# Optimization experiments

Measured on AMD Instinct MI355X. Metric: run time of the kernel, lower is better.

## Reference

```python
import jax, jax.numpy as jnp
import numpy as np

DELTA = 1.0
CENSORING_WEIGHT = 1.0
N = 16777216  # batch_size


def setup_inputs() -> dict:
    key = jax.random.key(0)
    k1, k2, k3, k4, k5, k6 = jax.random.split(key, 6)
    return {
        "pred_ecoli": jax.random.normal(k1, (N,), dtype=jnp.float32),
        "pred_saureus": jax.random.normal(k2, (N,), dtype=jnp.float32),
        "targets": jax.random.normal(k3, (N,), dtype=jnp.float32),
        "bacteria_ids": jax.random.randint(k4, (N,), 0, 2, dtype=jnp.int32),
        "is_censored": jax.random.bernoulli(k5, 0.5, (N,)),
        "censoring_threshold": jax.random.normal(k6, (N,), dtype=jnp.float32),
    }


def _huber(pred, target, delta):
    abs_error = jnp.abs(pred - target)
    quadratic = jnp.minimum(abs_error, delta)  # clamp(max=delta)
    linear = abs_error - quadratic
    return 0.5 * quadratic ** 2 + delta * linear


def reference(pred_ecoli, pred_saureus, targets, bacteria_ids, is_censored, censoring_threshold):
    # head selection: bacteria_id == 0 -> E.coli head, else S.aureus head
    pred = jnp.where(bacteria_ids == 0, pred_ecoli, pred_saureus)
    # censored branch: clamp(threshold - pred, min=0)^2 * censoring_weight
    censored_loss = CENSORING_WEIGHT * jnp.maximum(censoring_threshold - pred, 0.0) ** 2
    huber = _huber(pred, targets, DELTA)
    per_sample = jnp.where(is_censored, censored_loss, huber)
    return jnp.mean(per_sample)
```

## Files before the change

### kernel.cpp

```cpp
#include <hip/hip_runtime.h>

#define NBLOCKS 2048
#define NTHREADS 256

__device__ __forceinline__ float per_sample(float pe, float ps, float tg,
                                            float th, int bid, int cen) {
  float pred = (bid == 0) ? pe : ps;
  float d = fmaxf(th - pred, 0.0f);
  float closs = d * d;
  float ae = fabsf(pred - tg);
  float q = fminf(ae, 1.0f);
  float hub = 0.5f * q * q + (ae - q);
  return cen ? closs : hub;
}

__global__ void detect_layout(const unsigned char* __restrict__ cens,
                              int* __restrict__ flag) {
  __shared__ int any;
  if (threadIdx.x == 0) any = 0;
  __syncthreads();
  int local = 0;
  for (int i = threadIdx.x; i < 4096; i += blockDim.x) {
    if ((i & 3) != 0 && cens[i] != 0) local = 1;
  }
  if (local) atomicOr(&any, 1);
  __syncthreads();
  if (threadIdx.x == 0) *flag = (any == 0) ? 1 : 0;
}

__device__ __forceinline__ float proc4(const float4& e, const float4& s,
                                       const float4& t, const float4& h,
                                       const int4& b, int c0, int c1, int c2,
                                       int c3) {
  float a = per_sample(e.x, s.x, t.x, h.x, b.x, c0);
  a += per_sample(e.y, s.y, t.y, h.y, b.y, c1);
  a += per_sample(e.z, s.z, t.z, h.z, b.z, c2);
  a += per_sample(e.w, s.w, t.w, h.w, b.w, c3);
  return a;
}

__global__ __launch_bounds__(NTHREADS, 8) void dualhead_loss_kernel(
    const float4* __restrict__ pe, const float4* __restrict__ ps,
    const float4* __restrict__ tg, const int4* __restrict__ bid,
    const void* __restrict__ cens, const float4* __restrict__ th,
    const int* __restrict__ flag, float* __restrict__ partials, int nvec) {
  const int is32 = *flag;
  float acc = 0.0f;
  const int stride = gridDim.x * blockDim.x;
  int i = blockIdx.x * blockDim.x + threadIdx.x;

  for (; i + stride < nvec; i += 2 * stride) {
    const int j = i + stride;
    float4 e0 = pe[i], e1 = pe[j];
    float4 s0 = ps[i], s1 = ps[j];
    float4 t0 = tg[i], t1 = tg[j];
    float4 h0 = th[i], h1 = th[j];
    int4 b0 = bid[i], b1 = bid[j];
    int c00, c01, c02, c03, c10, c11, c12, c13;
    if (is32) {
      int4 c0 = ((const int4*)cens)[i];
      int4 c1 = ((const int4*)cens)[j];
      c00 = c0.x; c01 = c0.y; c02 = c0.z; c03 = c0.w;
      c10 = c1.x; c11 = c1.y; c12 = c1.z; c13 = c1.w;
    } else {
      uchar4 c0 = ((const uchar4*)cens)[i];
      uchar4 c1 = ((const uchar4*)cens)[j];
      c00 = c0.x; c01 = c0.y; c02 = c0.z; c03 = c0.w;
      c10 = c1.x; c11 = c1.y; c12 = c1.z; c13 = c1.w;
    }
    acc += proc4(e0, s0, t0, h0, b0, c00, c01, c02, c03);
    acc += proc4(e1, s1, t1, h1, b1, c10, c11, c12, c13);
  }
  for (; i < nvec; i += stride) {
    float4 e = pe[i], s = ps[i], t = tg[i], h = th[i];
    int4 b = bid[i];
    int c0, c1, c2, c3;
    if (is32) {
      int4 c = ((const int4*)cens)[i];
      c0 = c.x; c1 = c.y; c2 = c.z; c3 = c.w;
    } else {
      uchar4 c = ((const uchar4*)cens)[i];
      c0 = c.x; c1 = c.y; c2 = c.z; c3 = c.w;
    }
    acc += proc4(e, s, t, h, b, c0, c1, c2, c3);
  }

  for (int off = 32; off > 0; off >>= 1) acc += __shfl_down(acc, off, 64);
  __shared__ float wsum[NTHREADS / 64];
  const int lane = threadIdx.x & 63;
  const int wid = threadIdx.x >> 6;
  if (lane == 0) wsum[wid] = acc;
  __syncthreads();
  if (threadIdx.x == 0) {
    float b = 0.0f;
    for (int w = 0; w < NTHREADS / 64; ++w) b += wsum[w];
    partials[blockIdx.x] = b;
  }
}

__global__ void final_reduce(const float* __restrict__ partials, int n,
                             float* __restrict__ out, double inv_n) {
  double acc = 0.0;
  for (int i = threadIdx.x; i < n; i += blockDim.x) acc += (double)partials[i];
  for (int off = 32; off > 0; off >>= 1) acc += __shfl_down(acc, off, 64);
  __shared__ double wsum[256 / 64];
  const int lane = threadIdx.x & 63;
  const int wid = threadIdx.x >> 6;
  if (lane == 0) wsum[wid] = acc;
  __syncthreads();
  if (threadIdx.x == 0) {
    double s = 0.0;
    for (int w = 0; w < 4; ++w) s += wsum[w];
    out[0] = (float)(s * inv_n);
  }
}

extern "C" void kernel_launch(void* const* d_in, const int* in_sizes, int n_in,
                              void* d_out, int out_size, void* d_ws, size_t ws_size,
                              hipStream_t stream) {
  const float* pe = (const float*)d_in[0];
  const float* ps = (const float*)d_in[1];
  const float* tg = (const float*)d_in[2];
  const int* bid = (const int*)d_in[3];
  const void* cens = d_in[4];
  const float* th = (const float*)d_in[5];
  const int n = in_sizes[0];
  const int nvec = n / 4;

  float* partials = (float*)d_ws;
  int* flag = (int*)((char*)d_ws + NBLOCKS * sizeof(float));

  detect_layout<<<1, 256, 0, stream>>>((const unsigned char*)cens, flag);
  dualhead_loss_kernel<<<NBLOCKS, NTHREADS, 0, stream>>>(
      (const float4*)pe, (const float4*)ps, (const float4*)tg,
      (const int4*)bid, cens, (const float4*)th, flag, partials, nvec);
  final_reduce<<<1, 256, 0, stream>>>(partials, NBLOCKS, (float*)d_out,
                                      1.0 / (double)n);
}
```

Measured before the change: 87.22 us.

## Fuse layout detection and final reduction into single streaming kernel

Removes the separate layout-detection and final-reduce kernel launches. Each wavefront now probes the first 256 bytes of the censoring mask with a ballot to infer whether it is byte or int32 encoded. Block partials are summed with a double atomicAdd and a last-block counter that writes the mean. A memset replaces the launch that reset the workspace. Risks include atomic contention across 2048 blocks and a heuristic probe over only 256 bytes.

```diff
diff --git a/kernel.cpp b/kernel.cpp
--- a/kernel.cpp
+++ b/kernel.cpp
@@ -14,20 +14,6 @@
   return cen ? closs : hub;
 }
 
-__global__ void detect_layout(const unsigned char* __restrict__ cens,
-                              int* __restrict__ flag) {
-  __shared__ int any;
-  if (threadIdx.x == 0) any = 0;
-  __syncthreads();
-  int local = 0;
-  for (int i = threadIdx.x; i < 4096; i += blockDim.x) {
-    if ((i & 3) != 0 && cens[i] != 0) local = 1;
-  }
-  if (local) atomicOr(&any, 1);
-  __syncthreads();
-  if (threadIdx.x == 0) *flag = (any == 0) ? 1 : 0;
-}
-
 __device__ __forceinline__ float proc4(const float4& e, const float4& s,
                                        const float4& t, const float4& h,
                                        const int4& b, int c0, int c1, int c2,
@@ -39,12 +25,15 @@
   return a;
 }
 
-__global__ __launch_bounds__(NTHREADS, 8) void dualhead_loss_kernel(
+__global__ __launch_bounds__(NTHREADS, 8) void dualhead_fused_kernel(
     const float4* __restrict__ pe, const float4* __restrict__ ps,
     const float4* __restrict__ tg, const int4* __restrict__ bid,
     const void* __restrict__ cens, const float4* __restrict__ th,
-    const int* __restrict__ flag, float* __restrict__ partials, int nvec) {
-  const int is32 = *flag;
+    double* __restrict__ accum, unsigned* __restrict__ counter,
+    float* __restrict__ out, int nvec, double inv_n) {
+  unsigned probe = ((const unsigned*)cens)[threadIdx.x & 63];
+  const bool is8 = __ballot((probe & 0xFFFFFF00u) != 0) != 0ULL;
+
   float acc = 0.0f;
   const int stride = gridDim.x * blockDim.x;
   int i = blockIdx.x * blockDim.x + threadIdx.x;
@@ -57,14 +46,14 @@
     float4 h0 = th[i], h1 = th[j];
     int4 b0 = bid[i], b1 = bid[j];
     int c00, c01, c02, c03, c10, c11, c12, c13;
-    if (is32) {
-      int4 c0 = ((const int4*)cens)[i];
-      int4 c1 = ((const int4*)cens)[j];
+    if (is8) {
+      uchar4 c0 = ((const uchar4*)cens)[i];
+      uchar4 c1 = ((const uchar4*)cens)[j];
       c00 = c0.x; c01 = c0.y; c02 = c0.z; c03 = c0.w;
       c10 = c1.x; c11 = c1.y; c12 = c1.z; c13 = c1.w;
     } else {
-      uchar4 c0 = ((const uchar4*)cens)[i];
-      uchar4 c1 = ((const uchar4*)cens)[j];
+      int4 c0 = ((const int4*)cens)[i];
+      int4 c1 = ((const int4*)cens)[j];
       c00 = c0.x; c01 = c0.y; c02 = c0.z; c03 = c0.w;
       c10 = c1.x; c11 = c1.y; c12 = c1.z; c13 = c1.w;
     }
@@ -75,11 +64,11 @@
     float4 e = pe[i], s = ps[i], t = tg[i], h = th[i];
     int4 b = bid[i];
     int c0, c1, c2, c3;
-    if (is32) {
-      int4 c = ((const int4*)cens)[i];
+    if (is8) {
+      uchar4 c = ((const uchar4*)cens)[i];
       c0 = c.x; c1 = c.y; c2 = c.z; c3 = c.w;
     } else {
-      uchar4 c = ((const uchar4*)cens)[i];
+      int4 c = ((const int4*)cens)[i];
       c0 = c.x; c1 = c.y; c2 = c.z; c3 = c.w;
     }
     acc += proc4(e, s, t, h, b, c0, c1, c2, c3);
@@ -91,27 +80,18 @@
   const int wid = threadIdx.x >> 6;
   if (lane == 0) wsum[wid] = acc;
   __syncthreads();
+
   if (threadIdx.x == 0) {
     float b = 0.0f;
     for (int w = 0; w < NTHREADS / 64; ++w) b += wsum[w];
-    partials[blockIdx.x] = b;
-  }
-}
-
-__global__ void final_reduce(const float* __restrict__ partials, int n,
-                             float* __restrict__ out, double inv_n) {
-  double acc = 0.0;
-  for (int i = threadIdx.x; i < n; i += blockDim.x) acc += (double)partials[i];
-  for (int off = 32; off > 0; off >>= 1) acc += __shfl_down(acc, off, 64);
-  __shared__ double wsum[256 / 64];
-  const int lane = threadIdx.x & 63;
-  const int wid = threadIdx.x >> 6;
-  if (lane == 0) wsum[wid] = acc;
-  __syncthreads();
-  if (threadIdx.x == 0) {
-    double s = 0.0;
-    for (int w = 0; w < 4; ++w) s += wsum[w];
-    out[0] = (float)(s * inv_n);
+    atomicAdd(accum, (double)b);
+    __threadfence();
+    unsigned t = atomicAdd(counter, 1u);
+    if (t == gridDim.x - 1) {
+      __threadfence();
+      double s = atomicAdd(accum, 0.0);
+      out[0] = (float)(s * inv_n);
+    }
   }
 }
 
@@ -127,13 +107,13 @@
   const int n = in_sizes[0];
   const int nvec = n / 4;
 
-  float* partials = (float*)d_ws;
-  int* flag = (int*)((char*)d_ws + NBLOCKS * sizeof(float));
+  double* accum = (double*)d_ws;
+  unsigned* counter = (unsigned*)((char*)d_ws + sizeof(double));
 
-  detect_layout<<<1, 256, 0, stream>>>((const unsigned char*)cens, flag);
-  dualhead_loss_kernel<<<NBLOCKS, NTHREADS, 0, stream>>>(
+  hipMemsetAsync(d_ws, 0, 16, stream);
+
+  dualhead_fused_kernel<<<NBLOCKS, NTHREADS, 0, stream>>>(
       (const float4*)pe, (const float4*)ps, (const float4*)tg,
-      (const int4*)bid, cens, (const float4*)th, flag, partials, nvec);
-  final_reduce<<<1, 256, 0, stream>>>(partials, NBLOCKS, (float*)d_out,
-                                      1.0 / (double)n);
+      (const int4*)bid, cens, (const float4*)th, accum, counter,
+      (float*)d_out, nvec, 1.0 / (double)n);
 }
```

After: 175.3 us. 101% more time.

## Fold layout detection into main kernel and use contiguous per-block chunks

Applied to the files above, without the earlier changes.

Drops the separate detect_layout launch. Each wavefront of the main kernel now reads the first 64 words of the censor mask and uses a ballot to decide whether it holds bytes or 32-bit values. The main loop also changes from a grid-stride pattern to a contiguous chunk per block, with a leftover loop for the remainder. This removes one kernel launch and its serialization, at the cost of a small redundant probe read in every wave and a 256-byte detection window instead of 4096 bytes.

```diff
diff --git a/kernel.cpp b/kernel.cpp
--- a/kernel.cpp
+++ b/kernel.cpp
@@ -14,20 +14,6 @@
   return cen ? closs : hub;
 }
 
-__global__ void detect_layout(const unsigned char* __restrict__ cens,
-                              int* __restrict__ flag) {
-  __shared__ int any;
-  if (threadIdx.x == 0) any = 0;
-  __syncthreads();
-  int local = 0;
-  for (int i = threadIdx.x; i < 4096; i += blockDim.x) {
-    if ((i & 3) != 0 && cens[i] != 0) local = 1;
-  }
-  if (local) atomicOr(&any, 1);
-  __syncthreads();
-  if (threadIdx.x == 0) *flag = (any == 0) ? 1 : 0;
-}
-
 __device__ __forceinline__ float proc4(const float4& e, const float4& s,
                                        const float4& t, const float4& h,
                                        const int4& b, int c0, int c1, int c2,
@@ -39,47 +25,65 @@
   return a;
 }
 
-__global__ __launch_bounds__(NTHREADS, 8) void dualhead_loss_kernel(
+__global__ __launch_bounds__(NTHREADS, 8) void dualhead_main(
     const float4* __restrict__ pe, const float4* __restrict__ ps,
     const float4* __restrict__ tg, const int4* __restrict__ bid,
     const void* __restrict__ cens, const float4* __restrict__ th,
-    const int* __restrict__ flag, float* __restrict__ partials, int nvec) {
-  const int is32 = *flag;
+    float* __restrict__ partials, int nvec) {
+  unsigned probe = ((const unsigned*)cens)[threadIdx.x & 63];
+  const bool is8 = __ballot((probe & 0xFFFFFF00u) != 0) != 0ULL;
+
+  const int vpb = nvec / gridDim.x;
+  const int base = blockIdx.x * vpb;
+  const int end = base + vpb;
   float acc = 0.0f;
-  const int stride = gridDim.x * blockDim.x;
-  int i = blockIdx.x * blockDim.x + threadIdx.x;
+  int i = base + threadIdx.x;
 
-  for (; i + stride < nvec; i += 2 * stride) {
-    const int j = i + stride;
+  for (; i + NTHREADS < end; i += 2 * NTHREADS) {
+    const int j = i + NTHREADS;
     float4 e0 = pe[i], e1 = pe[j];
     float4 s0 = ps[i], s1 = ps[j];
     float4 t0 = tg[i], t1 = tg[j];
     float4 h0 = th[i], h1 = th[j];
     int4 b0 = bid[i], b1 = bid[j];
     int c00, c01, c02, c03, c10, c11, c12, c13;
-    if (is32) {
-      int4 c0 = ((const int4*)cens)[i];
-      int4 c1 = ((const int4*)cens)[j];
+    if (is8) {
+      uchar4 c0 = ((const uchar4*)cens)[i];
+      uchar4 c1 = ((const uchar4*)cens)[j];
       c00 = c0.x; c01 = c0.y; c02 = c0.z; c03 = c0.w;
       c10 = c1.x; c11 = c1.y; c12 = c1.z; c13 = c1.w;
     } else {
-      uchar4 c0 = ((const uchar4*)cens)[i];
-      uchar4 c1 = ((const uchar4*)cens)[j];
+      int4 c0 = ((const int4*)cens)[i];
+      int4 c1 = ((const int4*)cens)[j];
       c00 = c0.x; c01 = c0.y; c02 = c0.z; c03 = c0.w;
       c10 = c1.x; c11 = c1.y; c12 = c1.z; c13 = c1.w;
     }
     acc += proc4(e0, s0, t0, h0, b0, c00, c01, c02, c03);
     acc += proc4(e1, s1, t1, h1, b1, c10, c11, c12, c13);
   }
-  for (; i < nvec; i += stride) {
+  for (; i < end; i += NTHREADS) {
     float4 e = pe[i], s = ps[i], t = tg[i], h = th[i];
     int4 b = bid[i];
     int c0, c1, c2, c3;
-    if (is32) {
+    if (is8) {
+      uchar4 c = ((const uchar4*)cens)[i];
+      c0 = c.x; c1 = c.y; c2 = c.z; c3 = c.w;
+    } else {
       int4 c = ((const int4*)cens)[i];
       c0 = c.x; c1 = c.y; c2 = c.z; c3 = c.w;
+    }
+    acc += proc4(e, s, t, h, b, c0, c1, c2, c3);
+  }
+  for (int r = gridDim.x * vpb + blockIdx.x * NTHREADS + threadIdx.x; r < nvec;
+       r += gridDim.x * NTHREADS) {
+    float4 e = pe[r], s = ps[r], t = tg[r], h = th[r];
+    int4 b = bid[r];
+    int c0, c1, c2, c3;
+    if (is8) {
+      uchar4 c = ((const uchar4*)cens)[r];
+      c0 = c.x; c1 = c.y; c2 = c.z; c3 = c.w;
     } else {
-      uchar4 c = ((const uchar4*)cens)[i];
+      int4 c = ((const int4*)cens)[r];
       c0 = c.x; c1 = c.y; c2 = c.z; c3 = c.w;
     }
     acc += proc4(e, s, t, h, b, c0, c1, c2, c3);
@@ -128,12 +132,10 @@
   const int nvec = n / 4;
 
   float* partials = (float*)d_ws;
-  int* flag = (int*)((char*)d_ws + NBLOCKS * sizeof(float));
 
-  detect_layout<<<1, 256, 0, stream>>>((const unsigned char*)cens, flag);
-  dualhead_loss_kernel<<<NBLOCKS, NTHREADS, 0, stream>>>(
+  dualhead_main<<<NBLOCKS, NTHREADS, 0, stream>>>(
       (const float4*)pe, (const float4*)ps, (const float4*)tg,
-      (const int4*)bid, cens, (const float4*)th, flag, partials, nvec);
+      (const int4*)bid, cens, (const float4*)th, partials, nvec);
   final_reduce<<<1, 256, 0, stream>>>(partials, NBLOCKS, (float*)d_out,
                                       1.0 / (double)n);
 }
```

Result: faster. 73.97 us (-15.2%).
